# Optimization experiments

Measured on AMD Instinct MI355X. Metric: run time of the kernel, lower is better.

The kernel has to match this reference:

```python
import jax, jax.numpy as jnp
import numpy as np

COMMITMENT_COST = 0.25
EPS = 1e-10


def setup_inputs() -> dict:
    key = jax.random.key(0)
    k1, k2 = jax.random.split(key)
    x = jax.random.normal(k1, (64, 4096, 64), dtype=jnp.float32)          # [B, T, D]
    embedding = jax.random.normal(k2, (512, 64), dtype=jnp.float32)       # [K, D] codebook
    return {"x": x, "embedding": embedding}


def reference(x, embedding):
    B, T, D = x.shape
    K = embedding.shape[0]
    flat = x.reshape(-1, D)                                               # [N, D]
    N = flat.shape[0]

    distances = (jnp.sum(flat * flat, axis=1, keepdims=True)
                 - 2.0 * (flat @ embedding.T)
                 + jnp.sum(embedding * embedding, axis=1))

    idx = jnp.argmin(distances, axis=1)                                   # [N] nearest code
    quantized = embedding[idx].reshape(x.shape)                           # gather lookup

    # commitment loss (EMA variant: only e_latent_loss, codebook frozen w.r.t. loss)
    e_latent_loss = jnp.mean((jax.lax.stop_gradient(quantized) - x) ** 2)
    loss = COMMITMENT_COST * e_latent_loss

    # straight-through estimator
    q_st = x + jax.lax.stop_gradient(quantized - x)

    # perplexity via scatter-add histogram of code usage
    counts = jnp.zeros((K,), dtype=x.dtype).at[idx].add(jnp.ones((), x.dtype))
    avg_probs = counts / jnp.asarray(N, x.dtype)
    perplexity = jnp.exp(-jnp.sum(avg_probs * jnp.log(avg_probs + EPS)))

    return q_st, loss, perplexity
```

## Files before the change

### kernel.cpp

```cpp
#include <hip/hip_runtime.h>
#include <math.h>

#define N_ROWS   262144
#define DIM      64
#define KCODES   512
#define MT       64
#define NTHREADS 256
#define NBLOCKS  (N_ROWS / MT)
#define XS_STRIDE 68
#define ES_STRIDE 72
#define MARGIN   2e-3f

typedef float f32x4 __attribute__((ext_vector_type(4)));
typedef short s16x8 __attribute__((ext_vector_type(8)));


__device__ __forceinline__ unsigned short f2bf(float f) {
    unsigned u = __float_as_uint(f);
    unsigned r = u + 0x7fffu + ((u >> 16) & 1u);
    return (unsigned short)(r >> 16);
}
__device__ __forceinline__ float bf2f(unsigned short h) {
    return __uint_as_float(((unsigned)h) << 16);
}

__global__ __launch_bounds__(64) void vq_prep(const float* __restrict__ emb,
                                              float* __restrict__ esq,
                                              int* __restrict__ counts,
                                              float* __restrict__ lossAdj,
                                              unsigned short* __restrict__ eh,
                                              unsigned short* __restrict__ el) {
    int k = blockIdx.x * 64 + threadIdx.x;
    const float* e = emb + (size_t)k * DIM;
    float s = 0.f;
    #pragma unroll
    for (int d = 0; d < DIM; ++d) s += e[d] * e[d];
    esq[k] = s;
    counts[k] = 0;
    #pragma unroll
    for (int c8 = 0; c8 < 8; ++c8) {
        s16x8 h8, l8;
        #pragma unroll
        for (int j = 0; j < 8; ++j) {
            float v = e[c8 * 8 + j];
            unsigned short hb = f2bf(v);
            h8[j] = (short)hb;
            l8[j] = (short)f2bf(v - bf2f(hb));
        }
        *(s16x8*)&eh[k * DIM + c8 * 8] = h8;
        *(s16x8*)&el[k * DIM + c8 * 8] = l8;
    }
    if (k == 0) *lossAdj = 0.f;
}

__global__ __launch_bounds__(NTHREADS, 2) void vq_main(
    const float* __restrict__ x, const float* __restrict__ emb,
    const float* __restrict__ g_esq,
    const unsigned short* __restrict__ eh_g, const unsigned short* __restrict__ el_g,
    unsigned short* __restrict__ g_idx, float* __restrict__ g_lossPart,
    float* __restrict__ lossAdj, int* __restrict__ counts, float* __restrict__ out)
{
    __shared__ float xs[MT * XS_STRIDE];
    __shared__ unsigned short ehs[128 * ES_STRIDE];
    __shared__ unsigned short els[128 * ES_STRIDE];
    __shared__ float esq_s[KCODES];
    __shared__ int   idx_s[MT];
    __shared__ int   flg_s[MT];
    __shared__ int   flist[MT];
    __shared__ int   nflag;
    __shared__ float wred[4];

    const int tid  = threadIdx.x;
    const int R0   = blockIdx.x * MT;
    const int w    = tid >> 6;
    const int lane = tid & 63;
    const int m    = lane & 15;
    const int q    = lane >> 4;

    #pragma unroll
    for (int i = 0; i < 4; ++i) {
        int flat = tid + NTHREADS * i;
        int r  = flat >> 4;
        int qc = flat & 15;
        f32x4 v = *(const f32x4*)&x[(size_t)(R0 + r) * DIM + 4 * qc];
        *(f32x4*)&xs[r * XS_STRIDE + 4 * qc] = v;
    }
    esq_s[tid]       = g_esq[tid];
    esq_s[tid + 256] = g_esq[tid + 256];
    if (tid == 0) nflag = 0;
    __syncthreads();

    s16x8 axh[2], axl[2];
    const int lrow = w * 16 + m;
    #pragma unroll
    for (int kc = 0; kc < 2; ++kc) {
        const float* px = &xs[lrow * XS_STRIDE + kc * 32 + q * 8];
        s16x8 h, l;
        #pragma unroll
        for (int t = 0; t < 8; ++t) {
            float v = px[t];
            unsigned short hb = f2bf(v);
            h[t] = (short)hb;
            l[t] = (short)f2bf(v - bf2f(hb));
        }
        axh[kc] = h; axl[kc] = l;
    }

    f32x4 acc[32];
    #pragma unroll
    for (int a = 0; a < 32; ++a) acc[a] = (f32x4){0.f, 0.f, 0.f, 0.f};

    for (int c = 0; c < 4; ++c) {
        if (c) __syncthreads();
        #pragma unroll
        for (int i = 0; i < 4; ++i) {
            int ch = tid + NTHREADS * i;
            int rl = ch >> 3, off = (ch & 7) * 8;
            size_t gofs = (size_t)(c * 128 + rl) * DIM + off;
            *(s16x8*)&ehs[rl * ES_STRIDE + off] = *(const s16x8*)&eh_g[gofs];
            *(s16x8*)&els[rl * ES_STRIDE + off] = *(const s16x8*)&el_g[gofs];
        }
        __syncthreads();
        #pragma unroll
        for (int ct = 0; ct < 8; ++ct) {
            const int a = c * 8 + ct;
            #pragma unroll
            for (int kc = 0; kc < 2; ++kc) {
                const int bofs = (ct * 16 + m) * ES_STRIDE + kc * 32 + q * 8;
                s16x8 bh = *(const s16x8*)&ehs[bofs];
                s16x8 bl = *(const s16x8*)&els[bofs];
                acc[a] = __builtin_amdgcn_mfma_f32_16x16x32_bf16(axh[kc], bh, acc[a], 0, 0, 0);
                acc[a] = __builtin_amdgcn_mfma_f32_16x16x32_bf16(axl[kc], bh, acc[a], 0, 0, 0);
                acc[a] = __builtin_amdgcn_mfma_f32_16x16x32_bf16(axh[kc], bl, acc[a], 0, 0, 0);
            }
        }
    }

    float b1[4], b2[4]; int i1[4];
    #pragma unroll
    for (int r = 0; r < 4; ++r) { b1[r] = 3.4e38f; b2[r] = 3.4e38f; i1[r] = 0; }
    #pragma unroll
    for (int a = 0; a < 32; ++a) {
        int col = a * 16 + m;
        float e2 = esq_s[col];
        #pragma unroll
        for (int r = 0; r < 4; ++r) {
            float dist = e2 - 2.f * acc[a][r];
            if (dist < b1[r]) { b2[r] = b1[r]; b1[r] = dist; i1[r] = col; }
            else if (dist < b2[r]) b2[r] = dist;
        }
    }
    #pragma unroll
    for (int s = 1; s < 16; s <<= 1) {
        #pragma unroll
        for (int r = 0; r < 4; ++r) {
            float ob1 = __shfl_xor(b1[r], s);
            int   oi1 = __shfl_xor(i1[r], s);
            float ob2 = __shfl_xor(b2[r], s);
            bool owin = (ob1 < b1[r]) || (ob1 == b1[r] && oi1 < i1[r]);
            float lb1 = owin ? b1[r] : ob1;
            b2[r] = fminf(fminf(b2[r], ob2), lb1);
            if (owin) { b1[r] = ob1; i1[r] = oi1; }
        }
    }
    if (m == 0) {
        #pragma unroll
        for (int r = 0; r < 4; ++r) {
            int lrw = w * 16 + q * 4 + r;
            idx_s[lrw] = i1[r];
            flg_s[lrw] = (b2[r] - b1[r] < MARGIN) ? 1 : 0;
        }
    }
    __syncthreads();

    if (tid < MT) {
        if (flg_s[tid]) { int p = atomicAdd(&nflag, 1); flist[p] = tid; }
        else g_idx[R0 + tid] = (unsigned short)idx_s[tid];
    }

    const int r  = tid >> 2;
    const int d0 = (tid & 3) * 16;
    float lpart = 0.f;
    if (!flg_s[r]) {
        const int ki = idx_s[r];
        const float* erow = emb + (size_t)ki * DIM;
        #pragma unroll
        for (int s4 = 0; s4 < 4; ++s4) {
            int d = d0 + 4 * s4;
            f32x4 e4 = *(const f32x4*)&erow[d];
            float xv0 = xs[r * XS_STRIDE + d + 0];
            float xv1 = xs[r * XS_STRIDE + d + 1];
            float xv2 = xs[r * XS_STRIDE + d + 2];
            float xv3 = xs[r * XS_STRIDE + d + 3];
            float f0 = e4.x - xv0, f1 = e4.y - xv1, f2 = e4.z - xv2, f3 = e4.w - xv3;
            f32x4 o = {xv0 + f0, xv1 + f1, xv2 + f2, xv3 + f3};
            *(f32x4*)&out[(size_t)(R0 + r) * DIM + d] = o;
            lpart += f0*f0 + f1*f1 + f2*f2 + f3*f3;
        }
    }
    #pragma unroll
    for (int off = 32; off > 0; off >>= 1) lpart += __shfl_down(lpart, off);
    if ((tid & 63) == 0) wred[tid >> 6] = lpart;
    __syncthreads();
    if (tid == 0) g_lossPart[blockIdx.x] = wred[0] + wred[1] + wred[2] + wred[3];

    for (int fi = w; fi < nflag; fi += 4) {
        int lrw = flist[fi];
        int row = R0 + lrw;
        const float* xr = &x[(size_t)row * DIM];
        float best = 3.4e38f; int bidx = 0;
        #pragma unroll
        for (int j = 0; j < 8; ++j) {
            int cc = lane * 8 + j;
            const float* er = &emb[(size_t)cc * DIM];
            float dot = 0.f;
            #pragma unroll
            for (int d = 0; d < DIM; ++d) dot = fmaf(xr[d], er[d], dot);
            float dist = g_esq[cc] - 2.f * dot;
            if (dist < best) { best = dist; bidx = cc; }
        }
        #pragma unroll
        for (int s = 1; s < 64; s <<= 1) {
            float ob = __shfl_xor(best, s);
            int   oi = __shfl_xor(bidx, s);
            if (ob < best || (ob == best && oi < bidx)) { best = ob; bidx = oi; }
        }
        float xv = xr[lane];
        float ev = emb[(size_t)bidx * DIM + lane];
        float f  = ev - xv;
        out[(size_t)row * DIM + lane] = xv + f;
        float lp = f * f;
        #pragma unroll
        for (int s = 1; s < 64; s <<= 1) lp += __shfl_xor(lp, s);
        if (lane == 0) {
            atomicAdd(lossAdj, lp);
            g_idx[row] = (unsigned short)bidx;
            idx_s[lrw] = bidx;
        }
    }
    __syncthreads();

    if (tid < MT) atomicAdd(&counts[idx_s[tid]], 1);
}

__global__ __launch_bounds__(512) void vq_final(const int* __restrict__ counts,
                                                const float* __restrict__ lossPart,
                                                const float* __restrict__ lossAdj,
                                                float* __restrict__ out) {
    __shared__ float redp[8];
    __shared__ float redl[8];
    int k = threadIdx.x;
    float p = (float)counts[k] * (1.f / 262144.f);
    float t = p * logf(p + 1e-10f);
    float l = 0.f;
    #pragma unroll
    for (int i = 0; i < 8; ++i) l += lossPart[k + 512 * i];
    #pragma unroll
    for (int off = 32; off > 0; off >>= 1) {
        t += __shfl_down(t, off);
        l += __shfl_down(l, off);
    }
    if ((k & 63) == 0) { redp[k >> 6] = t; redl[k >> 6] = l; }
    __syncthreads();
    if (k == 0) {
        float s = 0.f, ls = 0.f;
        #pragma unroll
        for (int i = 0; i < 8; ++i) { s += redp[i]; ls += redl[i]; }
        out[16777216] = (ls + *lossAdj) * (0.25f / 16777216.f);
        out[16777217] = expf(-s);
    }
}

extern "C" void kernel_launch(void* const* d_in, const int* in_sizes, int n_in,
                              void* d_out, int out_size, void* d_ws, size_t ws_size,
                              hipStream_t stream) {
    const float* x   = (const float*)d_in[0];
    const float* emb = (const float*)d_in[1];
    float* out = (float*)d_out;

    char* ws = (char*)d_ws;
    float*          esq      = (float*)(ws + 0);
    int*            counts   = (int*)(ws + 2048);
    float*          lossAdj  = (float*)(ws + 4096);
    unsigned short* eh       = (unsigned short*)(ws + 4608);
    unsigned short* el       = (unsigned short*)(ws + 70144);
    unsigned short* gidx     = (unsigned short*)(ws + 168448);
    float*          lossPart = (float*)(ws + 692736);

    vq_prep<<<8, 64, 0, stream>>>(emb, esq, counts, lossAdj, eh, el);
    vq_main<<<NBLOCKS, NTHREADS, 0, stream>>>(x, emb, esq, eh, el,
                                              gidx, lossPart, lossAdj, counts, out);
    vq_final<<<1, 512, 0, stream>>>(counts, lossPart, lossAdj, out);
}
```

Measured before the change: 322.6 us.

## Defer near-tie exact rescoring and histogram to a separate tail kernel

The main kernel no longer rescores ambiguous rows or updates the global code histogram. Instead it sets a bit in a global mask for each near-tie row. A new 64-block tail kernel walks the mask and rescores flagged rows in fp32. It then builds per-block shared-memory histograms from the stored indices and has the last-arriving block compute loss and perplexity. This removes per-block tail imbalance and global count atomics from the main kernel, at the cost of re-reading the indices and an extra pass whose parallelism is limited to 64 blocks.

```diff
diff --git a/kernel.cpp b/kernel.cpp
--- a/kernel.cpp
+++ b/kernel.cpp
@@ -29,7 +29,9 @@
                                               int* __restrict__ counts,
                                               float* __restrict__ lossAdj,
                                               unsigned short* __restrict__ eh,
-                                              unsigned short* __restrict__ el) {
+                                              unsigned short* __restrict__ el,
+                                              unsigned* __restrict__ mask,
+                                              int* __restrict__ arrive) {
     int k = blockIdx.x * 64 + threadIdx.x;
     const float* e = emb + (size_t)k * DIM;
     float s = 0.f;
@@ -50,7 +52,9 @@
         *(s16x8*)&eh[k * DIM + c8 * 8] = h8;
         *(s16x8*)&el[k * DIM + c8 * 8] = l8;
     }
-    if (k == 0) *lossAdj = 0.f;
+    #pragma unroll
+    for (int i = 0; i < 16; ++i) mask[k * 16 + i] = 0u;
+    if (k == 0) { *lossAdj = 0.f; *arrive = 0; }
 }
 
 __global__ __launch_bounds__(NTHREADS, 2) void vq_main(
@@ -58,7 +62,7 @@
     const float* __restrict__ g_esq,
     const unsigned short* __restrict__ eh_g, const unsigned short* __restrict__ el_g,
     unsigned short* __restrict__ g_idx, float* __restrict__ g_lossPart,
-    float* __restrict__ lossAdj, int* __restrict__ counts, float* __restrict__ out)
+    unsigned* __restrict__ g_mask, float* __restrict__ out)
 {
     __shared__ float xs[MT * XS_STRIDE];
     __shared__ unsigned short ehs[128 * ES_STRIDE];
@@ -66,8 +70,6 @@
     __shared__ float esq_s[KCODES];
     __shared__ int   idx_s[MT];
     __shared__ int   flg_s[MT];
-    __shared__ int   flist[MT];
-    __shared__ int   nflag;
     __shared__ float wred[4];
 
     const int tid  = threadIdx.x;
@@ -87,7 +89,6 @@
     }
     esq_s[tid]       = g_esq[tid];
     esq_s[tid + 256] = g_esq[tid + 256];
-    if (tid == 0) nflag = 0;
     __syncthreads();
 
     s16x8 axh[2], axl[2];
@@ -168,15 +169,16 @@
         for (int r = 0; r < 4; ++r) {
             int lrw = w * 16 + q * 4 + r;
             idx_s[lrw] = i1[r];
-            flg_s[lrw] = (b2[r] - b1[r] < MARGIN) ? 1 : 0;
-        }
-    }
-    __syncthreads();
-
-    if (tid < MT) {
-        if (flg_s[tid]) { int p = atomicAdd(&nflag, 1); flist[p] = tid; }
-        else g_idx[R0 + tid] = (unsigned short)idx_s[tid];
-    }
+            int f = (b2[r] - b1[r] < MARGIN) ? 1 : 0;
+            flg_s[lrw] = f;
+            if (f) {
+                int grow = R0 + lrw;
+                atomicOr(&g_mask[grow >> 5], 1u << (grow & 31));
+            }
+        }
+    }
+    __syncthreads();
+    if (tid < MT) g_idx[R0 + tid] = (unsigned short)idx_s[tid];
 
     const int r  = tid >> 2;
     const int d0 = (tid & 3) * 16;
@@ -203,56 +205,87 @@
     if ((tid & 63) == 0) wred[tid >> 6] = lpart;
     __syncthreads();
     if (tid == 0) g_lossPart[blockIdx.x] = wred[0] + wred[1] + wred[2] + wred[3];
-
-    for (int fi = w; fi < nflag; fi += 4) {
-        int lrw = flist[fi];
-        int row = R0 + lrw;
-        const float* xr = &x[(size_t)row * DIM];
-        float best = 3.4e38f; int bidx = 0;
-        #pragma unroll
-        for (int j = 0; j < 8; ++j) {
-            int cc = lane * 8 + j;
-            const float* er = &emb[(size_t)cc * DIM];
-            float dot = 0.f;
-            #pragma unroll
-            for (int d = 0; d < DIM; ++d) dot = fmaf(xr[d], er[d], dot);
-            float dist = g_esq[cc] - 2.f * dot;
-            if (dist < best) { best = dist; bidx = cc; }
-        }
-        #pragma unroll
-        for (int s = 1; s < 64; s <<= 1) {
-            float ob = __shfl_xor(best, s);
-            int   oi = __shfl_xor(bidx, s);
-            if (ob < best || (ob == best && oi < bidx)) { best = ob; bidx = oi; }
-        }
-        float xv = xr[lane];
-        float ev = emb[(size_t)bidx * DIM + lane];
-        float f  = ev - xv;
-        out[(size_t)row * DIM + lane] = xv + f;
-        float lp = f * f;
-        #pragma unroll
-        for (int s = 1; s < 64; s <<= 1) lp += __shfl_xor(lp, s);
-        if (lane == 0) {
-            atomicAdd(lossAdj, lp);
-            g_idx[row] = (unsigned short)bidx;
-            idx_s[lrw] = bidx;
-        }
-    }
-    __syncthreads();
-
-    if (tid < MT) atomicAdd(&counts[idx_s[tid]], 1);
-}
-
-__global__ __launch_bounds__(512) void vq_final(const int* __restrict__ counts,
-                                                const float* __restrict__ lossPart,
-                                                const float* __restrict__ lossAdj,
-                                                float* __restrict__ out) {
+}
+
+__global__ __launch_bounds__(512) void vq_tail(
+    const float* __restrict__ x, const float* __restrict__ emb,
+    const float* __restrict__ g_esq, unsigned short* __restrict__ g_idx,
+    float* __restrict__ lossAdj, const unsigned* __restrict__ g_mask,
+    int* __restrict__ counts, const float* __restrict__ lossPart,
+    int* __restrict__ arrive, float* __restrict__ out)
+{
+    __shared__ int   h[KCODES];
     __shared__ float redp[8];
     __shared__ float redl[8];
-    int k = threadIdx.x;
-    float p = (float)counts[k] * (1.f / 262144.f);
-    float t = p * logf(p + 1e-10f);
-    float l = 0.f;
+    __shared__ int   lastBlk;
+
+    const int tid  = threadIdx.x;
+    const int wv   = tid >> 6;
+    const int lane = tid & 63;
+    const int b    = blockIdx.x;
+
+    h[tid & (KCODES - 1)] = 0;
+
+    #pragma unroll 1
+    for (int wd = 0; wd < 16; ++wd) {
+        const int word = b * 128 + wv * 16 + wd;
+        unsigned mw = g_mask[word];
+        while (mw) {
+            int bit = __ffs(mw) - 1;
+            mw &= mw - 1;
+            int row = word * 32 + bit;
+            const float* xr = &x[(size_t)row * DIM];
+            float best = 3.4e38f; int bidx = 0;
+            #pragma unroll
+            for (int j = 0; j < 8; ++j) {
+                int c = lane * 8 + j;
+                const float* er = &emb[(size_t)c * DIM];
+                float dot = 0.f;
+                #pragma unroll
+                for (int d = 0; d < DIM; ++d) dot = fmaf(xr[d], er[d], dot);
+                float dist = g_esq[c] - 2.f * dot;
+                if (dist < best) { best = dist; bidx = c; }
+            }
+            #pragma unroll
+            for (int s = 1; s < 64; s <<= 1) {
+                float ob = __shfl_xor(best, s);
+                int   oi = __shfl_xor(bidx, s);
+                if (ob < best || (ob == best && oi < bidx)) { best = ob; bidx = oi; }
+            }
+            float xv = xr[lane];
+            float ev = emb[(size_t)bidx * DIM + lane];
+            float f  = ev - xv;
+            out[(size_t)row * DIM + lane] = xv + f;
+            float lp = f * f;
+            #pragma unroll
+            for (int s = 1; s < 64; s <<= 1) lp += __shfl_xor(lp, s);
+            if (lane == 0) {
+                atomicAdd(lossAdj, lp);
+                g_idx[row] = (unsigned short)bidx;
+            }
+        }
+    }
+    __threadfence_block();
+    __syncthreads();
+
+    const unsigned short* p = g_idx + (size_t)b * 4096;
+    #pragma unroll
+    for (int i = 0; i < 8; ++i)
+        atomicAdd(&h[p[tid + 512 * i]], 1);
+    __syncthreads();
+    int hv = h[tid];
+    if (hv) atomicAdd(&counts[tid], hv);
+
+    __threadfence();
+    if (tid == 0) lastBlk = (atomicAdd(arrive, 1) == 63) ? 1 : 0;
+    __syncthreads();
+    if (!lastBlk) return;
+    __threadfence();
+
+    int k = tid;
+    float pp = (float)atomicAdd(&counts[k], 0) * (1.f / 262144.f);
+    float t  = pp * logf(pp + 1e-10f);
+    float l  = 0.f;
     #pragma unroll
     for (int i = 0; i < 8; ++i) l += lossPart[k + 512 * i];
     #pragma unroll
@@ -266,7 +299,8 @@
         float s = 0.f, ls = 0.f;
         #pragma unroll
         for (int i = 0; i < 8; ++i) { s += redp[i]; ls += redl[i]; }
-        out[16777216] = (ls + *lossAdj) * (0.25f / 16777216.f);
+        float adj = atomicAdd(lossAdj, 0.f);
+        out[16777216] = (ls + adj) * (0.25f / 16777216.f);
         out[16777217] = expf(-s);
     }
 }
@@ -282,13 +316,16 @@
     float*          esq      = (float*)(ws + 0);
     int*            counts   = (int*)(ws + 2048);
     float*          lossAdj  = (float*)(ws + 4096);
+    int*            arrive   = (int*)(ws + 4100);
     unsigned short* eh       = (unsigned short*)(ws + 4608);
     unsigned short* el       = (unsigned short*)(ws + 70144);
+    unsigned*       mask     = (unsigned*)(ws + 135680);
     unsigned short* gidx     = (unsigned short*)(ws + 168448);
     float*          lossPart = (float*)(ws + 692736);
 
-    vq_prep<<<8, 64, 0, stream>>>(emb, esq, counts, lossAdj, eh, el);
+    vq_prep<<<8, 64, 0, stream>>>(emb, esq, counts, lossAdj, eh, el, mask, arrive);
     vq_main<<<NBLOCKS, NTHREADS, 0, stream>>>(x, emb, esq, eh, el,
-                                              gidx, lossPart, lossAdj, counts, out);
-    vq_final<<<1, 512, 0, stream>>>(counts, lossPart, lossAdj, out);
-}
+                                              gidx, lossPart, mask, out);
+    vq_tail<<<64, 512, 0, stream>>>(x, emb, esq, gidx, lossAdj, mask,
+                                    counts, lossPart, arrive, out);
+}
```

Measured after the change: 324.6 us. No clear change (+0.6%).
